# Kernel tuning notes

Hardware: AMD Instinct MI355X
Metric: run time of the kernel (lower is better)

## Reference

```python
import jax, jax.numpy as jnp
import numpy as np

NUM_HEADS = 4
NUM_GROUPS = 8
EPS = 1e-5


def setup_inputs() -> dict:
    key = jax.random.key(0)
    ks = jax.random.split(key, 4)
    B, C, H, W = 4, 256, 64, 64
    x = jax.random.normal(ks[0], (B, C, H, W), dtype=jnp.float32)
    gn_w = jnp.ones((C,), dtype=jnp.float32)
    gn_b = jnp.zeros((C,), dtype=jnp.float32)
    # 1x1 convs == per-pixel matmuls; store kernels as [out_ch, in_ch]
    w_qkv = jax.random.normal(ks[1], (3 * C, C), dtype=jnp.float32) * (1.0 / np.sqrt(C))
    b_qkv = jnp.zeros((3 * C,), dtype=jnp.float32)
    w_proj = jax.random.normal(ks[2], (C, C), dtype=jnp.float32) * (1.0 / np.sqrt(C))
    b_proj = jnp.zeros((C,), dtype=jnp.float32)
    return {"x": x, "gn_w": gn_w, "gn_b": gn_b, "w_qkv": w_qkv,
            "b_qkv": b_qkv, "w_proj": w_proj, "b_proj": b_proj}


def reference(x, gn_w, gn_b, w_qkv, b_qkv, w_proj, b_proj):
    B, C, H, W = x.shape
    N = H * W
    nh = NUM_HEADS
    dh = C // nh

    # GroupNorm(8, C)
    xg = x.reshape(B, NUM_GROUPS, C // NUM_GROUPS, N)
    mu = jnp.mean(xg, axis=(2, 3), keepdims=True)
    var = jnp.var(xg, axis=(2, 3), keepdims=True)
    h = ((xg - mu) * jax.lax.rsqrt(var + EPS)).reshape(B, C, N)
    h = h * gn_w[None, :, None] + gn_b[None, :, None]

    # qkv 1x1 conv
    qkv = jnp.einsum('oc,bcn->bon', w_qkv, h) + b_qkv[None, :, None]
    q, k, v = jnp.split(qkv, 3, axis=1)  # each [B, C, N]
    q = q.reshape(B, nh, dh, N)
    k = k.reshape(B, nh, dh, N)
    v = v.reshape(B, nh, dh, N)

    # attn = softmax(q^T k / sqrt(dh)) over last dim -> [B, nh, N, N]
    scores = jnp.einsum('bhdi,bhdj->bhij', q, k) / jnp.sqrt(jnp.array(dh, dtype=x.dtype))
    attn = jax.nn.softmax(scores, axis=-1)

    # out = attn @ v^T, back to channel-major layout
    out = jnp.einsum('bhij,bhdj->bhdi', attn, v).reshape(B, C, N)

    # proj_out 1x1 conv + residual
    out = jnp.einsum('oc,bcn->bon', w_proj, out) + b_proj[None, :, None]
    return x + out.reshape(B, C, H, W)
```

## Files before the change

### kernel.cpp

```cpp
#include <hip/hip_runtime.h>
#include <math.h>

#define N_PIX 4096
#define C_CH  256
#define NH    4
#define DH    64

typedef __attribute__((ext_vector_type(8))) short bf16x8;
typedef __attribute__((ext_vector_type(4))) float f32x4;

static __device__ __forceinline__ unsigned short f2bf(float f) {
  union { float f; unsigned u; } v; v.f = f;
  unsigned r = v.u + 0x7fffu + ((v.u >> 16) & 1u);
  return (unsigned short)(r >> 16);
}
static __device__ __forceinline__ unsigned pk2(float a, float b) {
  return (unsigned)f2bf(a) | ((unsigned)f2bf(b) << 16);
}
static __device__ __forceinline__ unsigned pk2t(float a, float b) {
  return __builtin_amdgcn_perm(__float_as_uint(b), __float_as_uint(a),
                               0x07060302u);
}
#if __has_builtin(__builtin_amdgcn_exp2f)
#define EXP2(x) __builtin_amdgcn_exp2f(x)
#else
#define EXP2(x) exp2f(x)
#endif
static __device__ __forceinline__ int swz(int row, int g) {
  return (row << 6) + ((((row >> 2) ^ row ^ g) & 7) << 3);
}

__global__ __launch_bounds__(256) void gn_part_kernel(
    const float* __restrict__ x, const float* __restrict__ wqkv,
    const float* __restrict__ wproj, float* __restrict__ part,
    unsigned short* __restrict__ wB) {
  const int g = blockIdx.x, b = blockIdx.y, z = blockIdx.z;
  const int t = threadIdx.x;
  {
    const int bid = blockIdx.z * 32 + blockIdx.y * 8 + blockIdx.x;
    const int i = bid * 256 + t;
    const float* src = (i < 49152) ? (wqkv + (size_t)i * 4)
                                   : (wproj + (size_t)(i - 49152) * 4);
    float4 v = *(const float4*)src;
    uint2 u;
    u.x = pk2(v.x, v.y);
    u.y = pk2(v.z, v.w);
    *(uint2*)(wB + (size_t)i * 4) = u;
  }
  const float* base = x + (size_t)(b * C_CH + g * 32 + z * 4) * N_PIX;
  float sum = 0.f, sq = 0.f;
  for (int i = t * 4; i < 4 * N_PIX; i += 256 * 4) {
    float4 v = *(const float4*)(base + i);
    sum += v.x + v.y + v.z + v.w;
    sq  += v.x * v.x + v.y * v.y + v.z * v.z + v.w * v.w;
  }
  for (int off = 32; off >= 1; off >>= 1) {
    sum += __shfl_down(sum, off, 64);
    sq  += __shfl_down(sq,  off, 64);
  }
  __shared__ float ps[4], pq[4];
  if ((t & 63) == 0) { ps[t >> 6] = sum; pq[t >> 6] = sq; }
  __syncthreads();
  if (t == 0) {
    int idx = ((b * 8 + g) * 8 + z) * 2;
    part[idx + 0] = ps[0] + ps[1] + ps[2] + ps[3];
    part[idx + 1] = pq[0] + pq[1] + pq[2] + pq[3];
  }
}

__global__ __launch_bounds__(256) void gn_apply_kernel(
    const float* __restrict__ x, const float* __restrict__ part,
    const float* __restrict__ gn_w, const float* __restrict__ gn_b,
    unsigned short* __restrict__ hT) {
  const int n0 = blockIdx.x * 64;
  const int c0 = blockIdx.y * 64;
  const int b  = blockIdx.z;
  const int t  = threadIdx.x;
  __shared__ unsigned short Ht[64 * 64];
  __shared__ float ls[64], lsh[64];
  if (t < 64) {
    int c = c0 + t;
    int g = c >> 5;
    float S = 0.f, Q = 0.f;
#pragma unroll
    for (int z = 0; z < 8; ++z) {
      int idx = ((b * 8 + g) * 8 + z) * 2;
      S += part[idx + 0];
      Q += part[idx + 1];
    }
    const float inv_cnt = 1.f / (32.f * N_PIX);
    float mu  = S * inv_cnt;
    float var = Q * inv_cnt - mu * mu;
    float rstd = rsqrtf(var + 1e-5f);
    float s = rstd * gn_w[c];
    ls[t]  = s;
    lsh[t] = gn_b[c] - mu * s;
  }
  __syncthreads();
  const int cl = t >> 4;
  const int nl = (t & 15) * 4;
#pragma unroll
  for (int r = 0; r < 4; ++r) {
    int ce = cl + r * 16;
    float sv = ls[ce], sh = lsh[ce];
    float4 v =
        *(const float4*)(x + ((size_t)(b * C_CH + c0 + ce)) * N_PIX + n0 + nl);
#pragma unroll
    for (int i = 0; i < 4; ++i) {
      float f = ((const float*)&v)[i] * sv + sh;
      Ht[swz(nl + i, ce >> 3) + (ce & 7)] = f2bf(f);
    }
  }
  __syncthreads();
  {
    const int row = t >> 2, sg = (t & 3) * 2;
    uint4 o0 = *(const uint4*)&Ht[swz(row, sg + 0)];
    uint4 o1 = *(const uint4*)&Ht[swz(row, sg + 1)];
    size_t go = ((size_t)(b * N_PIX + n0 + row)) * C_CH + c0 + sg * 8;
    *(uint4*)(hT + go) = o0;
    *(uint4*)(hT + go + 8) = o1;
  }
}

__global__ __launch_bounds__(256) void qkv_gemm_kernel(
    const unsigned short* __restrict__ hT, const unsigned short* __restrict__ wB,
    const float* __restrict__ bqkv, unsigned short* __restrict__ qT,
    unsigned short* __restrict__ kT, unsigned short* __restrict__ vO) {
  const int mb = blockIdx.x, type = mb >> 2, head = mb & 3;
  const int n0 = blockIdx.y * 128;
  const int b  = blockIdx.z;
  const int t  = threadIdx.x;
  const int wave = t >> 6, lane = t & 63, quad = lane >> 4, lc = lane & 15;

  __shared__ unsigned short Ws[64 * 64];
  __shared__ unsigned short Hs[128 * 64];

  f32x4 acc[4][2];
#pragma unroll
  for (int i = 0; i < 4; ++i)
#pragma unroll
    for (int j = 0; j < 2; ++j) acc[i][j] = (f32x4){0.f, 0.f, 0.f, 0.f};

  const int wrow = t >> 2, wgb = (t & 3) * 2;
  const int hrow = t >> 1, hgb = (t & 1) * 4;
  const unsigned short* wp = wB + (size_t)(mb * 64 + wrow) * C_CH;
  const unsigned short* ap =
      hT + ((size_t)(b * N_PIX + n0 + hrow)) * C_CH + hgb * 8;

  for (int k0 = 0; k0 < C_CH; k0 += 64) {
    __syncthreads();
    {
      const unsigned short* s0 = wp + k0 + wgb * 8;
      uint4 u0 = *(const uint4*)(s0);
      uint4 u1 = *(const uint4*)(s0 + 8);
      *(uint4*)&Ws[swz(wrow, wgb + 0)] = u0;
      *(uint4*)&Ws[swz(wrow, wgb + 1)] = u1;
    }
    {
      const unsigned short* s0 = ap + k0;
#pragma unroll
      for (int j = 0; j < 4; ++j) {
        uint4 u = *(const uint4*)(s0 + j * 8);
        *(uint4*)&Hs[swz(hrow, hgb + j)] = u;
      }
    }
    __syncthreads();
#pragma unroll
    for (int kh = 0; kh < 2; ++kh) {
      bf16x8 wf[4], hf[2];
#pragma unroll
      for (int mt = 0; mt < 4; ++mt)
        wf[mt] = *(const bf16x8*)&Ws[swz(mt * 16 + lc, kh * 4 + quad)];
#pragma unroll
      for (int nt = 0; nt < 2; ++nt)
        hf[nt] = *(const bf16x8*)&Hs[swz(wave * 32 + nt * 16 + lc, kh * 4 + quad)];
      if (type < 2) {
#pragma unroll
        for (int mt = 0; mt < 4; ++mt)
#pragma unroll
          for (int nt = 0; nt < 2; ++nt)
            acc[mt][nt] = __builtin_amdgcn_mfma_f32_16x16x32_bf16(
                wf[mt], hf[nt], acc[mt][nt], 0, 0, 0);
      } else {
#pragma unroll
        for (int mt = 0; mt < 4; ++mt)
#pragma unroll
          for (int nt = 0; nt < 2; ++nt)
            acc[mt][nt] = __builtin_amdgcn_mfma_f32_16x16x32_bf16(
                hf[nt], wf[mt], acc[mt][nt], 0, 0, 0);
      }
    }
  }

  if (type < 2) {
    unsigned short* dst = (type == 0) ? qT : kT;
    const float qs = (type == 0) ? 0.125f * 1.44269504f : 1.0f;
#pragma unroll
    for (int mt = 0; mt < 4; ++mt)
#pragma unroll
      for (int nt = 0; nt < 2; ++nt) {
        int n = n0 + wave * 32 + nt * 16 + lc;
        int d0 = mt * 16 + quad * 4;
        float b0 = bqkv[mb * 64 + d0 + 0], b1 = bqkv[mb * 64 + d0 + 1];
        float b2 = bqkv[mb * 64 + d0 + 2], b3 = bqkv[mb * 64 + d0 + 3];
        uint2 w;
        w.x = pk2((acc[mt][nt][0] + b0) * qs, (acc[mt][nt][1] + b1) * qs);
        w.y = pk2((acc[mt][nt][2] + b2) * qs, (acc[mt][nt][3] + b3) * qs);
        *(uint2*)(dst + ((size_t)((b * NH + head) * N_PIX + n)) * 64 + d0) = w;
      }
  } else {
#pragma unroll
    for (int mt = 0; mt < 4; ++mt)
#pragma unroll
      for (int nt = 0; nt < 2; ++nt) {
        int d = mt * 16 + lc;
        float bias = bqkv[mb * 64 + d];
        int pix = n0 + wave * 32 + nt * 16 + quad * 4;
        uint2 w;
        w.x = pk2(acc[mt][nt][0] + bias, acc[mt][nt][1] + bias);
        w.y = pk2(acc[mt][nt][2] + bias, acc[mt][nt][3] + bias);
        *(uint2*)(vO + ((size_t)((b * NH + head) * 64 + d)) * N_PIX + pix) = w;
      }
  }
}

__global__ __launch_bounds__(256) void attn_kernel(
    const unsigned short* __restrict__ qT, const unsigned short* __restrict__ kT,
    const unsigned short* __restrict__ vO, unsigned short* __restrict__ aT) {
  const int t  = threadIdx.x;
  const int i0 = blockIdx.x * 128;
  const int h  = blockIdx.y;
  const int b  = blockIdx.z;
  const size_t bh = (size_t)(b * NH + h);
  const unsigned short* qp = qT + bh * N_PIX * 64;
  const unsigned short* kp = kT + bh * N_PIX * 64;
  const unsigned short* vp = vO + bh * 64 * N_PIX;

  __shared__ unsigned short Qt[128 * 64];
  __shared__ unsigned short Kt[2 * 64 * 64];
  __shared__ unsigned short Vs[2 * 64 * 64];
  unsigned short* const Ps = Qt;

  const int wave = t >> 6, lane = t & 63, quad = lane >> 4, lc = lane & 15;
  const int qb0 = wave * 32, qb1 = wave * 32 + 16;
  const int srow = t >> 2, sg = (t & 3) * 2;
  const int qrow = t >> 1, qg = (t & 1) * 4;

  {
    const unsigned short* sp = qp + (size_t)(i0 + qrow) * 64 + qg * 8;
#pragma unroll
    for (int i = 0; i < 4; ++i) {
      uint4 u = *(const uint4*)(sp + i * 8);
      *(uint4*)&Qt[swz(qrow, qg + i)] = u;
    }
  }
  __syncthreads();
  bf16x8 aq[2][2];
  aq[0][0] = *(const bf16x8*)&Qt[swz(qb0 + lc, quad)];
  aq[0][1] = *(const bf16x8*)&Qt[swz(qb0 + lc, quad + 4)];
  aq[1][0] = *(const bf16x8*)&Qt[swz(qb1 + lc, quad)];
  aq[1][1] = *(const bf16x8*)&Qt[swz(qb1 + lc, quad + 4)];

  int kof0[4], kof1[4], vof0[4], vof1[4], pw[2][4];
#pragma unroll
  for (int jt = 0; jt < 4; ++jt) {
    kof0[jt] = swz(jt * 16 + lc, quad);
    kof1[jt] = swz(jt * 16 + lc, quad + 4);
    pw[0][jt] = swz(qb0 + lc, jt * 2 + (quad >> 1)) + (quad & 1) * 4;
    pw[1][jt] = swz(qb1 + lc, jt * 2 + (quad >> 1)) + (quad & 1) * 4;
  }
#pragma unroll
  for (int mt = 0; mt < 4; ++mt) {
    vof0[mt] = swz(mt * 16 + lc, quad);
    vof1[mt] = swz(mt * 16 + lc, quad + 4);
  }
  const int pb00 = swz(qb0 + lc, quad), pb01 = swz(qb0 + lc, quad + 4);
  const int pb10 = swz(qb1 + lc, quad), pb11 = swz(qb1 + lc, quad + 4);
  const int sw0 = swz(srow, sg + 0), sw1 = swz(srow, sg + 1);
  const unsigned short* kbase = kp + (size_t)srow * 64 + sg * 8;
  const unsigned short* vbase = vp + (size_t)srow * N_PIX + sg * 8;

  float la0 = 0.f, la1 = 0.f;
  f32x4 od[2][4];
#pragma unroll
  for (int qh = 0; qh < 2; ++qh)
#pragma unroll
    for (int mt = 0; mt < 4; ++mt) od[qh][mt] = (f32x4){0.f, 0.f, 0.f, 0.f};

  {
    uint4 k0 = *(const uint4*)(kbase);
    uint4 k1 = *(const uint4*)(kbase + 8);
    uint4 v0 = *(const uint4*)(vbase);
    uint4 v1 = *(const uint4*)(vbase + 8);
    *(uint4*)&Kt[sw0] = k0;
    *(uint4*)&Kt[sw1] = k1;
    *(uint4*)&Vs[sw0] = v0;
    *(uint4*)&Vs[sw1] = v1;
  }
  __syncthreads();

  {
    uint4 pk0 = *(const uint4*)(kbase + 4096);
    uint4 pk1 = *(const uint4*)(kbase + 4096 + 8);
    uint4 pv0 = *(const uint4*)(vbase + 64);
    uint4 pv1 = *(const uint4*)(vbase + 64 + 8);
#pragma unroll
    for (int jt = 0; jt < 4; ++jt) {
      bf16x8 bk0 = *(const bf16x8*)&Kt[kof0[jt]];
      bf16x8 bk1 = *(const bf16x8*)&Kt[kof1[jt]];
      f32x4 a0 = (f32x4){0.f, 0.f, 0.f, 0.f};
      a0 = __builtin_amdgcn_mfma_f32_16x16x32_bf16(bk0, aq[0][0], a0, 0, 0, 0);
      a0 = __builtin_amdgcn_mfma_f32_16x16x32_bf16(bk1, aq[0][1], a0, 0, 0, 0);
      f32x4 a1 = (f32x4){0.f, 0.f, 0.f, 0.f};
      a1 = __builtin_amdgcn_mfma_f32_16x16x32_bf16(bk0, aq[1][0], a1, 0, 0, 0);
      a1 = __builtin_amdgcn_mfma_f32_16x16x32_bf16(bk1, aq[1][1], a1, 0, 0, 0);
      float e0 = EXP2(a0[0]), e1 = EXP2(a0[1]), e2 = EXP2(a0[2]),
            e3 = EXP2(a0[3]);
      la0 += (e0 + e1) + (e2 + e3);
      uint2 u0;
      u0.x = pk2t(e0, e1);
      u0.y = pk2t(e2, e3);
      *(uint2*)&Ps[pw[0][jt]] = u0;
      float f0 = EXP2(a1[0]), f1 = EXP2(a1[1]), f2 = EXP2(a1[2]),
            f3 = EXP2(a1[3]);
      la1 += (f0 + f1) + (f2 + f3);
      uint2 u1;
      u1.x = pk2t(f0, f1);
      u1.y = pk2t(f2, f3);
      *(uint2*)&Ps[pw[1][jt]] = u1;
    }
    *(uint4*)&Kt[4096 + sw0] = pk0;
    *(uint4*)&Kt[4096 + sw1] = pk1;
    *(uint4*)&Vs[4096 + sw0] = pv0;
    *(uint4*)&Vs[4096 + sw1] = pv1;
  }

  for (int it = 1; it < 64; ++it) {
    const int cb = (it & 1) << 12;
    const int ob = 4096 - cb;
    __syncthreads();
    const size_t kadv = (size_t)((it + 1) & 63) * 4096;
    const size_t vadv = (size_t)((it + 1) & 63) * 64;
    uint4 pk0 = *(const uint4*)(kbase + kadv);
    uint4 pk1 = *(const uint4*)(kbase + kadv + 8);
    uint4 pv0 = *(const uint4*)(vbase + vadv);
    uint4 pv1 = *(const uint4*)(vbase + vadv + 8);

    f32x4 s0[4], s1[4];
#pragma unroll
    for (int jt = 0; jt < 4; ++jt) {
      bf16x8 bk0 = *(const bf16x8*)&Kt[cb + kof0[jt]];
      bf16x8 bk1 = *(const bf16x8*)&Kt[cb + kof1[jt]];
      f32x4 a0 = (f32x4){0.f, 0.f, 0.f, 0.f};
      a0 = __builtin_amdgcn_mfma_f32_16x16x32_bf16(bk0, aq[0][0], a0, 0, 0, 0);
      a0 = __builtin_amdgcn_mfma_f32_16x16x32_bf16(bk1, aq[0][1], a0, 0, 0, 0);
      f32x4 a1 = (f32x4){0.f, 0.f, 0.f, 0.f};
      a1 = __builtin_amdgcn_mfma_f32_16x16x32_bf16(bk0, aq[1][0], a1, 0, 0, 0);
      a1 = __builtin_amdgcn_mfma_f32_16x16x32_bf16(bk1, aq[1][1], a1, 0, 0, 0);
      s0[jt] = a0;
      s1[jt] = a1;
    }

    bf16x8 bp00 = *(const bf16x8*)&Ps[pb00];
    bf16x8 bp01 = *(const bf16x8*)&Ps[pb01];
    bf16x8 bp10 = *(const bf16x8*)&Ps[pb10];
    bf16x8 bp11 = *(const bf16x8*)&Ps[pb11];

#pragma unroll
    for (int mt = 0; mt < 4; ++mt) {
      bf16x8 av0 = *(const bf16x8*)&Vs[ob + vof0[mt]];
      bf16x8 av1 = *(const bf16x8*)&Vs[ob + vof1[mt]];
      od[0][mt] =
          __builtin_amdgcn_mfma_f32_16x16x32_bf16(av0, bp00, od[0][mt], 0, 0, 0);
      od[0][mt] =
          __builtin_amdgcn_mfma_f32_16x16x32_bf16(av1, bp01, od[0][mt], 0, 0, 0);
      od[1][mt] =
          __builtin_amdgcn_mfma_f32_16x16x32_bf16(av0, bp10, od[1][mt], 0, 0, 0);
      od[1][mt] =
          __builtin_amdgcn_mfma_f32_16x16x32_bf16(av1, bp11, od[1][mt], 0, 0, 0);
      float e0 = EXP2(s0[mt][0]), e1 = EXP2(s0[mt][1]), e2 = EXP2(s0[mt][2]),
            e3 = EXP2(s0[mt][3]);
      la0 += (e0 + e1) + (e2 + e3);
      uint2 u0;
      u0.x = pk2t(e0, e1);
      u0.y = pk2t(e2, e3);
      *(uint2*)&Ps[pw[0][mt]] = u0;
      float f0 = EXP2(s1[mt][0]), f1 = EXP2(s1[mt][1]), f2 = EXP2(s1[mt][2]),
            f3 = EXP2(s1[mt][3]);
      la1 += (f0 + f1) + (f2 + f3);
      uint2 u1;
      u1.x = pk2t(f0, f1);
      u1.y = pk2t(f2, f3);
      *(uint2*)&Ps[pw[1][mt]] = u1;
    }

    __syncthreads();
    *(uint4*)&Kt[ob + sw0] = pk0;
    *(uint4*)&Kt[ob + sw1] = pk1;
    *(uint4*)&Vs[ob + sw0] = pv0;
    *(uint4*)&Vs[ob + sw1] = pv1;
  }

  {
    bf16x8 bp00 = *(const bf16x8*)&Ps[pb00];
    bf16x8 bp01 = *(const bf16x8*)&Ps[pb01];
    bf16x8 bp10 = *(const bf16x8*)&Ps[pb10];
    bf16x8 bp11 = *(const bf16x8*)&Ps[pb11];
#pragma unroll
    for (int mt = 0; mt < 4; ++mt) {
      bf16x8 av0 = *(const bf16x8*)&Vs[4096 + vof0[mt]];
      bf16x8 av1 = *(const bf16x8*)&Vs[4096 + vof1[mt]];
      od[0][mt] =
          __builtin_amdgcn_mfma_f32_16x16x32_bf16(av0, bp00, od[0][mt], 0, 0, 0);
      od[0][mt] =
          __builtin_amdgcn_mfma_f32_16x16x32_bf16(av1, bp01, od[0][mt], 0, 0, 0);
      od[1][mt] =
          __builtin_amdgcn_mfma_f32_16x16x32_bf16(av0, bp10, od[1][mt], 0, 0, 0);
      od[1][mt] =
          __builtin_amdgcn_mfma_f32_16x16x32_bf16(av1, bp11, od[1][mt], 0, 0, 0);
    }
  }

  la0 += __shfl_xor(la0, 16, 64);
  la0 += __shfl_xor(la0, 32, 64);
  la1 += __shfl_xor(la1, 16, 64);
  la1 += __shfl_xor(la1, 32, 64);
  float inv0 = 1.f / la0;
  float inv1 = 1.f / la1;

#pragma unroll
  for (int mt = 0; mt < 4; ++mt) {
    uint2 u0, u1;
    u0.x = pk2(od[0][mt][0] * inv0, od[0][mt][1] * inv0);
    u0.y = pk2(od[0][mt][2] * inv0, od[0][mt][3] * inv0);
    u1.x = pk2(od[1][mt][0] * inv1, od[1][mt][1] * inv1);
    u1.y = pk2(od[1][mt][2] * inv1, od[1][mt][3] * inv1);
    *(uint2*)&Ps[swz(qb0 + lc, mt * 2 + (quad >> 1)) + (quad & 1) * 4] = u0;
    *(uint2*)&Ps[swz(qb1 + lc, mt * 2 + (quad >> 1)) + (quad & 1) * 4] = u1;
  }
  __syncthreads();
  {
    size_t go = ((size_t)(b * N_PIX + i0 + qrow)) * C_CH + h * 64 + qg * 8;
#pragma unroll
    for (int i = 0; i < 4; ++i) {
      uint4 o = *(const uint4*)&Ps[swz(qrow, qg + i)];
      *(uint4*)(aT + go + i * 8) = o;
    }
  }
}

__global__ __launch_bounds__(256) void proj_gemm_kernel(
    const unsigned short* __restrict__ aT, const unsigned short* __restrict__ wPB,
    const float* __restrict__ bproj, const float* __restrict__ x,
    float* __restrict__ out) {
  const int m0 = blockIdx.x * 64;
  const int n0 = blockIdx.y * 128;
  const int b  = blockIdx.z;
  const int t  = threadIdx.x;
  const int wave = t >> 6, lane = t & 63, quad = lane >> 4, lc = lane & 15;

  __shared__ unsigned short Ws[64 * 64];
  __shared__ unsigned short Hs[128 * 64];

  f32x4 acc[4][2];
#pragma unroll
  for (int i = 0; i < 4; ++i)
#pragma unroll
    for (int j = 0; j < 2; ++j) acc[i][j] = (f32x4){0.f, 0.f, 0.f, 0.f};

  const int wrow = t >> 2, wgb = (t & 3) * 2;
  const int hrow = t >> 1, hgb = (t & 1) * 4;
  const unsigned short* wp = wPB + (size_t)(m0 + wrow) * C_CH;
  const unsigned short* ap =
      aT + ((size_t)(b * N_PIX + n0 + hrow)) * C_CH + hgb * 8;

  for (int k0 = 0; k0 < C_CH; k0 += 64) {
    __syncthreads();
    {
      const unsigned short* s0 = wp + k0 + wgb * 8;
      uint4 u0 = *(const uint4*)(s0);
      uint4 u1 = *(const uint4*)(s0 + 8);
      *(uint4*)&Ws[swz(wrow, wgb + 0)] = u0;
      *(uint4*)&Ws[swz(wrow, wgb + 1)] = u1;
    }
    {
      const unsigned short* s0 = ap + k0;
#pragma unroll
      for (int j = 0; j < 4; ++j) {
        uint4 u = *(const uint4*)(s0 + j * 8);
        *(uint4*)&Hs[swz(hrow, hgb + j)] = u;
      }
    }
    __syncthreads();
#pragma unroll
    for (int kh = 0; kh < 2; ++kh) {
      bf16x8 wf[4], hf[2];
#pragma unroll
      for (int mt = 0; mt < 4; ++mt)
        wf[mt] = *(const bf16x8*)&Ws[swz(mt * 16 + lc, kh * 4 + quad)];
#pragma unroll
      for (int nt = 0; nt < 2; ++nt)
        hf[nt] = *(const bf16x8*)&Hs[swz(wave * 32 + nt * 16 + lc, kh * 4 + quad)];
#pragma unroll
      for (int mt = 0; mt < 4; ++mt)
#pragma unroll
        for (int nt = 0; nt < 2; ++nt)
          acc[mt][nt] = __builtin_amdgcn_mfma_f32_16x16x32_bf16(
              wf[mt], hf[nt], acc[mt][nt], 0, 0, 0);
    }
  }
#pragma unroll
  for (int mt = 0; mt < 4; ++mt) {
#pragma unroll
    for (int nt = 0; nt < 2; ++nt) {
      int n = n0 + wave * 32 + nt * 16 + lc;
#pragma unroll
      for (int r = 0; r < 4; ++r) {
        int c = m0 + mt * 16 + quad * 4 + r;
        size_t gi = ((size_t)(b * C_CH + c)) * N_PIX + n;
        out[gi] = acc[mt][nt][r] + bproj[c] + x[gi];
      }
    }
  }
}

extern "C" void kernel_launch(void* const* d_in, const int* in_sizes, int n_in,
                              void* d_out, int out_size, void* d_ws,
                              size_t ws_size, hipStream_t stream) {
  const float* x      = (const float*)d_in[0];
  const float* gn_w   = (const float*)d_in[1];
  const float* gn_b   = (const float*)d_in[2];
  const float* w_qkv  = (const float*)d_in[3];
  const float* b_qkv  = (const float*)d_in[4];
  const float* w_proj = (const float*)d_in[5];
  const float* b_proj = (const float*)d_in[6];
  float* out = (float*)d_out;

  float* ws   = (float*)d_ws;
  float* part = ws + 2048;
  unsigned short* qT = (unsigned short*)(ws + 4096);
  unsigned short* kT = qT + (size_t)4194304;
  unsigned short* vO = kT + (size_t)4194304;
  unsigned short* aT = vO + (size_t)4194304;
  unsigned short* hT = aT + (size_t)4194304;
  unsigned short* wB = hT + (size_t)4194304;
  unsigned short* wPB = wB + (size_t)49152 * 4;

  gn_part_kernel<<<dim3(8, 4, 8), dim3(256), 0, stream>>>(x, w_qkv, w_proj,
                                                          part, wB);
  gn_apply_kernel<<<dim3(64, 4, 4), dim3(256), 0, stream>>>(x, part, gn_w,
                                                            gn_b, hT);
  qkv_gemm_kernel<<<dim3(12, 32, 4), dim3(256), 0, stream>>>(
      hT, wB, b_qkv, qT, kT, vO);
  attn_kernel<<<dim3(32, 4, 4), dim3(256), 0, stream>>>(qT, kT, vO, aT);
  proj_gemm_kernel<<<dim3(4, 32, 4), dim3(256), 0, stream>>>(
      aT, wPB, b_proj, x, out);
}
```

Measured before the change: 214.9 us.

## Compute Q, K and V for one head per block to reuse staged activations

The QKV GEMM now gives each block all three projections (Q, K, V) of a head rather than one. The activation tile in shared memory is loaded once and reused across three weight tiles, which cuts global reads of hT threefold. The cost is 24 accumulator vectors per thread, more register and LDS pressure, and a grid reduced from 1536 to 512 blocks, which lowers occupancy and parallelism on a large GPU.

```diff
diff --git a/kernel.cpp b/kernel.cpp
--- a/kernel.cpp
+++ b/kernel.cpp
@@ -126,99 +126,117 @@
     const unsigned short* __restrict__ hT, const unsigned short* __restrict__ wB,
     const float* __restrict__ bqkv, unsigned short* __restrict__ qT,
     unsigned short* __restrict__ kT, unsigned short* __restrict__ vO) {
-  const int mb = blockIdx.x, type = mb >> 2, head = mb & 3;
+  const int head = blockIdx.x;
   const int n0 = blockIdx.y * 128;
   const int b  = blockIdx.z;
   const int t  = threadIdx.x;
   const int wave = t >> 6, lane = t & 63, quad = lane >> 4, lc = lane & 15;
 
-  __shared__ unsigned short Ws[64 * 64];
+  __shared__ unsigned short Ws[3 * 64 * 64];
   __shared__ unsigned short Hs[128 * 64];
 
-  f32x4 acc[4][2];
-#pragma unroll
-  for (int i = 0; i < 4; ++i)
-#pragma unroll
-    for (int j = 0; j < 2; ++j) acc[i][j] = (f32x4){0.f, 0.f, 0.f, 0.f};
+  f32x4 acc[3][4][2];
+#pragma unroll
+  for (int ty = 0; ty < 3; ++ty)
+#pragma unroll
+    for (int i = 0; i < 4; ++i)
+#pragma unroll
+      for (int j = 0; j < 2; ++j) acc[ty][i][j] = (f32x4){0.f, 0.f, 0.f, 0.f};
 
   const int wrow = t >> 2, wgb = (t & 3) * 2;
   const int hrow = t >> 1, hgb = (t & 1) * 4;
-  const unsigned short* wp = wB + (size_t)(mb * 64 + wrow) * C_CH;
+  const unsigned short* wp =
+      wB + (size_t)(head * 64 + wrow) * C_CH + wgb * 8;
   const unsigned short* ap =
       hT + ((size_t)(b * N_PIX + n0 + hrow)) * C_CH + hgb * 8;
-
-  for (int k0 = 0; k0 < C_CH; k0 += 64) {
+  const int wsw0 = swz(wrow, wgb + 0), wsw1 = swz(wrow, wgb + 1);
+  int hsw[4];
+#pragma unroll
+  for (int j = 0; j < 4; ++j) hsw[j] = swz(hrow, hgb + j);
+
+  for (int kc = 0; kc < 4; ++kc) {
+    const int k0 = kc * 64;
     __syncthreads();
-    {
-      const unsigned short* s0 = wp + k0 + wgb * 8;
+#pragma unroll
+    for (int ty = 0; ty < 3; ++ty) {
+      const unsigned short* s0 = wp + (size_t)ty * 256 * C_CH + k0;
       uint4 u0 = *(const uint4*)(s0);
       uint4 u1 = *(const uint4*)(s0 + 8);
-      *(uint4*)&Ws[swz(wrow, wgb + 0)] = u0;
-      *(uint4*)&Ws[swz(wrow, wgb + 1)] = u1;
+      *(uint4*)&Ws[ty * 4096 + wsw0] = u0;
+      *(uint4*)&Ws[ty * 4096 + wsw1] = u1;
     }
     {
       const unsigned short* s0 = ap + k0;
 #pragma unroll
       for (int j = 0; j < 4; ++j) {
         uint4 u = *(const uint4*)(s0 + j * 8);
-        *(uint4*)&Hs[swz(hrow, hgb + j)] = u;
+        *(uint4*)&Hs[hsw[j]] = u;
       }
     }
     __syncthreads();
 #pragma unroll
     for (int kh = 0; kh < 2; ++kh) {
-      bf16x8 wf[4], hf[2];
-#pragma unroll
-      for (int mt = 0; mt < 4; ++mt)
-        wf[mt] = *(const bf16x8*)&Ws[swz(mt * 16 + lc, kh * 4 + quad)];
+      bf16x8 hf[2];
 #pragma unroll
       for (int nt = 0; nt < 2; ++nt)
         hf[nt] = *(const bf16x8*)&Hs[swz(wave * 32 + nt * 16 + lc, kh * 4 + quad)];
-      if (type < 2) {
+#pragma unroll
+      for (int ty = 0; ty < 3; ++ty) {
+        bf16x8 wf[4];
 #pragma unroll
         for (int mt = 0; mt < 4; ++mt)
-#pragma unroll
-          for (int nt = 0; nt < 2; ++nt)
-            acc[mt][nt] = __builtin_amdgcn_mfma_f32_16x16x32_bf16(
-                wf[mt], hf[nt], acc[mt][nt], 0, 0, 0);
-      } else {
-#pragma unroll
-        for (int mt = 0; mt < 4; ++mt)
-#pragma unroll
-          for (int nt = 0; nt < 2; ++nt)
-            acc[mt][nt] = __builtin_amdgcn_mfma_f32_16x16x32_bf16(
-                hf[nt], wf[mt], acc[mt][nt], 0, 0, 0);
+          wf[mt] =
+              *(const bf16x8*)&Ws[ty * 4096 + swz(mt * 16 + lc, kh * 4 + quad)];
+        if (ty < 2) {
+#pragma unroll
+          for (int mt = 0; mt < 4; ++mt)
+#pragma unroll
+            for (int nt = 0; nt < 2; ++nt)
+              acc[ty][mt][nt] = __builtin_amdgcn_mfma_f32_16x16x32_bf16(
+                  wf[mt], hf[nt], acc[ty][mt][nt], 0, 0, 0);
+        } else {
+#pragma unroll
+          for (int mt = 0; mt < 4; ++mt)
+#pragma unroll
+            for (int nt = 0; nt < 2; ++nt)
+              acc[2][mt][nt] = __builtin_amdgcn_mfma_f32_16x16x32_bf16(
+                  hf[nt], wf[mt], acc[2][mt][nt], 0, 0, 0);
+        }
       }
     }
   }
 
-  if (type < 2) {
-    unsigned short* dst = (type == 0) ? qT : kT;
-    const float qs = (type == 0) ? 0.125f * 1.44269504f : 1.0f;
+#pragma unroll
+  for (int ty = 0; ty < 2; ++ty) {
+    unsigned short* dst = (ty == 0) ? qT : kT;
+    const float qs = (ty == 0) ? 0.125f * 1.44269504f : 1.0f;
+    const int bb = ty * 256 + head * 64;
 #pragma unroll
     for (int mt = 0; mt < 4; ++mt)
 #pragma unroll
       for (int nt = 0; nt < 2; ++nt) {
         int n = n0 + wave * 32 + nt * 16 + lc;
         int d0 = mt * 16 + quad * 4;
-        float b0 = bqkv[mb * 64 + d0 + 0], b1 = bqkv[mb * 64 + d0 + 1];
-        float b2 = bqkv[mb * 64 + d0 + 2], b3 = bqkv[mb * 64 + d0 + 3];
+        float b0 = bqkv[bb + d0 + 0], b1 = bqkv[bb + d0 + 1];
+        float b2 = bqkv[bb + d0 + 2], b3 = bqkv[bb + d0 + 3];
         uint2 w;
-        w.x = pk2((acc[mt][nt][0] + b0) * qs, (acc[mt][nt][1] + b1) * qs);
-        w.y = pk2((acc[mt][nt][2] + b2) * qs, (acc[mt][nt][3] + b3) * qs);
+        w.x = pk2((acc[ty][mt][nt][0] + b0) * qs, (acc[ty][mt][nt][1] + b1) * qs);
+        w.y = pk2((acc[ty][mt][nt][2] + b2) * qs, (acc[ty][mt][nt][3] + b3) * qs);
         *(uint2*)(dst + ((size_t)((b * NH + head) * N_PIX + n)) * 64 + d0) = w;
       }
-  } else {
+  }
+  {
+    const int bb = 512 + head * 64;
 #pragma unroll
     for (int mt = 0; mt < 4; ++mt)
 #pragma unroll
       for (int nt = 0; nt < 2; ++nt) {
         int d = mt * 16 + lc;
-        float bias = bqkv[mb * 64 + d];
+        float bias = bqkv[bb + d];
         int pix = n0 + wave * 32 + nt * 16 + quad * 4;
         uint2 w;
-        w.x = pk2(acc[mt][nt][0] + bias, acc[mt][nt][1] + bias);
-        w.y = pk2(acc[mt][nt][2] + bias, acc[mt][nt][3] + bias);
+        w.x = pk2(acc[2][mt][nt][0] + bias, acc[2][mt][nt][1] + bias);
+        w.y = pk2(acc[2][mt][nt][2] + bias, acc[2][mt][nt][3] + bias);
         *(uint2*)(vO + ((size_t)((b * NH + head) * 64 + d)) * N_PIX + pix) = w;
       }
   }
@@ -550,7 +568,7 @@
                                                           part, wB);
   gn_apply_kernel<<<dim3(64, 4, 4), dim3(256), 0, stream>>>(x, part, gn_w,
                                                             gn_b, hT);
-  qkv_gemm_kernel<<<dim3(12, 32, 4), dim3(256), 0, stream>>>(
+  qkv_gemm_kernel<<<dim3(4, 32, 4), dim3(256), 0, stream>>>(
       hT, wB, b_qkv, qT, kT, vO);
   attn_kernel<<<dim3(32, 4, 4), dim3(256), 0, stream>>>(qT, kT, vO, aT);
   proj_gemm_kernel<<<dim3(4, 32, 4), dim3(256), 0, stream>>>(
```

New measurement: 209.9 us. 1.02x faster.
